# Kernel tuning notes

Measured on AMD Instinct MI355X. Metric: run time of the kernel, lower is better.

## Reference

```python
import jax, jax.numpy as jnp
import numpy as np
from jax import lax

B, N, T, E, HE, HD, NE = 512, 100, 100, 128, 64, 256, 512
BETA = 0.25


def setup_inputs() -> dict:
    key = jax.random.key(0)
    ks = jax.random.split(key, 16)
    f32 = jnp.float32
    x = jax.random.normal(ks[0], (B, N, T), f32)
    traj_mask = (jax.random.uniform(ks[1], (B, N, T)) > 0.1).astype(f32)
    instance_mask = (jax.random.uniform(ks[2], (B, N)) > 0.2).astype(f32)

    def w_init(k, shape, fan_in):
        return (jax.random.normal(k, shape, f32) / np.sqrt(fan_in)).astype(f32)

    params = dict(
        conv1_w=w_init(ks[3], (HE, 2, 3), 2 * 3), conv1_b=jnp.zeros((HE,), f32),
        conv2_w=w_init(ks[4], (HE, HE, 3), HE * 3), conv2_b=jnp.zeros((HE,), f32),
        lat_w=w_init(ks[5], (E, HE), HE), lat_b=jnp.zeros((E,), f32),
        codebook=(jax.random.uniform(ks[6], (NE, E), f32) * 2.0 - 1.0) / NE,
        d1_w=w_init(ks[7], (HD, E), E), d1_b=jnp.zeros((HD,), f32),
        d2_w=w_init(ks[8], (HD, HD), HD), d2_b=jnp.zeros((HD,), f32),
        d3_w=w_init(ks[9], (T, HD), HD), d3_b=jnp.zeros((T,), f32),
    )
    return {"x": x, "traj_mask": traj_mask, "instance_mask": instance_mask, **params}


def _conv1d(h, w, b):
    # h: (M, C_in, L), w: (C_out, C_in, K) -> (M, C_out, L), padding=1 == SAME for K=3
    y = lax.conv_general_dilated(h, w, (1,), 'SAME', dimension_numbers=('NCH', 'OIH', 'NCH'))
    return jax.nn.relu(y + b[None, :, None])


def reference(x, traj_mask, instance_mask, conv1_w, conv1_b, conv2_w, conv2_b,
              lat_w, lat_b, codebook, d1_w, d1_b, d2_w, d2_b, d3_w, d3_b):
    b, n, t = x.shape
    steps = t // 2
    im = instance_mask[..., None]  # (B,N,1)

    # ---- encode (masked input) ----
    x_in = x * traj_mask * im
    h = x_in.reshape(b * n, steps, 2).transpose(0, 2, 1)  # (M, 2, steps)
    h = _conv1d(h, conv1_w, conv1_b)
    h = _conv1d(h, conv2_w, conv2_b)
    h = h.mean(axis=-1)                                   # (M, HE)
    z = (h @ lat_w.T + lat_b).reshape(b, n, -1)           # (B, N, E)
    z = z * im

    # ---- vector quantize (nbooks=1), quant_prop=1.0 ----
    zf = z.reshape(-1, z.shape[-1])                       # (M, E)
    d = ((zf * zf).sum(-1, keepdims=True)
         - 2.0 * zf @ codebook.T
         + (codebook * codebook).sum(-1))                 # (M, NE)
    idx = jnp.argmin(d, axis=-1)                          # (M,)
    zq = codebook[idx]                                    # (M, E) gather
    sg = lax.stop_gradient
    vq_loss = (BETA * jnp.mean((zf - sg(zq)) ** 2, -1)
               + jnp.mean((sg(zf) - zq) ** 2, -1)).reshape(b, n)
    zq = zf + sg(zq - zf)                                 # straight-through
    z_q = zq.reshape(b, n, -1)

    # ---- apply instance mask to VQ outputs ----
    denom = jnp.maximum(instance_mask.sum(), 1.0)
    vq_reduced = (vq_loss * instance_mask).sum() / denom
    indices = idx.reshape(b, n, 1)
    indices = jnp.where(im > 0, indices, jnp.full_like(indices, -1))
    z_q = z_q * im

    # ---- decode ----
    h2 = jax.nn.relu(z_q.reshape(b * n, -1) @ d1_w.T + d1_b)
    h2 = jax.nn.relu(h2 @ d2_w.T + d2_b)
    x_hat = (h2 @ d3_w.T + d3_b).reshape(b, n, t)

    # ---- masked reconstruction loss ----
    recon_w = im * traj_mask
    recon_loss = (((x_hat - x) ** 2) * recon_w).sum() / jnp.maximum(recon_w.sum(), 1.0)
    return x_hat, recon_loss, vq_reduced, indices
```

## Files before the change

### kernel.cpp

```cpp
#include <hip/hip_runtime.h>
#include <stdint.h>

typedef unsigned long long u64;
typedef unsigned short ushort_t;
typedef __attribute__((ext_vector_type(8))) short short8;
typedef __attribute__((ext_vector_type(8))) _Float16 half8;
typedef __attribute__((ext_vector_type(16))) float f32x16;


#define WS_RNP0     0ll
#define WS_RNP1     51200ll
#define WS_ZHI      102400ll
#define WS_ZLO      3379200ll
#define WS_ENCBHI   6656000ll
#define WS_ENCBLO   6662144ll
#define WS_CBHI     6668288ll
#define WS_CBLO     6701056ll
#define WS_CBNORM   6733824ll
#define WS_D1F      6734336ll
#define WS_D2F      6750720ll
#define WS_D3F      6783488ll
#define WS_ACCUMS   6799872ll
#define WS_GBEST    6799880ll
#define WS_RED      6902280ll

__device__ __host__ inline ushort_t bf16_rn(float v) {
  unsigned u = __float_as_uint(v);
  unsigned r = (u + 0x7fffu + ((u >> 16) & 1u)) >> 16;
  return (ushort_t)r;
}
union h2u { _Float16 h; unsigned short u; };
union s2h { short8 s; half8 h; };

__device__ inline unsigned pk2_bf16(float a, float b) {
  unsigned r;
  asm("v_cvt_pk_bf16_f32 %0, %1, %2" : "=v"(r) : "v"(a), "v"(b));
  return r;
}

__device__ inline int rowfn(int r, int half) { return (r & 3) + 8*(r >> 2) + 4*half; }

#define MFMA_BF16 __builtin_amdgcn_mfma_f32_32x32x16_bf16

__global__ __launch_bounds__(256) void prep_kernel(
    const float* __restrict__ w2, const float* __restrict__ cb,
    const float* __restrict__ d1w, const float* __restrict__ d2w,
    const float* __restrict__ d3w,
    ushort_t* __restrict__ ebhi, ushort_t* __restrict__ eblo,
    ushort_t* __restrict__ cbhi, ushort_t* __restrict__ cblo,
    ushort_t* __restrict__ d1f, ushort_t* __restrict__ d2f,
    ushort_t* __restrict__ d3f, float* __restrict__ cbnorm)
{
  const int total = 12288 + 65536 + 32768 + 65536 + 32768 + 512;
  for (int i = blockIdx.x*256 + threadIdx.x; i < total; i += gridDim.x*256) {
    int idx = i;
    if (idx < 12288) {
      int j = idx & 7, l6 = (idx >> 3) & 63, f = idx >> 9;
      int kt = f & 3, ntt = (f >> 2) & 1, t = f >> 3;
      int oc = ntt*32 + (l6 & 31);
      int ic = kt*16 + (l6 >> 5)*8 + j;
      float v = w2[(oc*64 + ic)*3 + t];
      ushort_t hi = bf16_rn(v);
      float hf = __uint_as_float(((unsigned)hi) << 16);
      ebhi[idx] = hi; eblo[idx] = bf16_rn(v - hf); continue;
    }
    idx -= 12288;
    if (idx < 65536) {
      int j = idx & 7, l6 = (idx >> 3) & 63, f = idx >> 9;
      int kt = f & 7, ntg = f >> 3;
      int k = kt*16 + (l6 >> 5)*8 + j;
      int n = ntg*32 + (l6 & 31);
      float v = cb[n*128 + k] * 512.0f;
      h2u a, b; a.h = (_Float16)v;
      b.h = (_Float16)(v - (float)a.h);
      cbhi[idx] = a.u; cblo[idx] = b.u; continue;
    }
    idx -= 65536;
    if (idx < 32768) {
      int j = idx & 7, l6 = (idx >> 3) & 63, f = idx >> 9;
      int kt = f & 7, ntg = f >> 3;
      int k = kt*16 + (l6 >> 5)*8 + j;
      int n = ntg*32 + (l6 & 31);
      d1f[idx] = bf16_rn(d1w[n*128 + k]); continue;
    }
    idx -= 32768;
    if (idx < 65536) {
      int j = idx & 7, l6 = (idx >> 3) & 63, f = idx >> 9;
      int kt = f & 15, ntg = f >> 4;
      int k = kt*16 + (l6 >> 5)*8 + j;
      int n = ntg*32 + (l6 & 31);
      d2f[idx] = bf16_rn(d2w[n*256 + k]); continue;
    }
    idx -= 65536;
    if (idx < 32768) {
      int j = idx & 7, l6 = (idx >> 3) & 63, f = idx >> 9;
      int kt = f & 15, ntg = f >> 4;
      int k = kt*16 + (l6 >> 5)*8 + j;
      int n = ntg*32 + (l6 & 31);
      d3f[idx] = (n < 100) ? bf16_rn(d3w[n*256 + k]) : (ushort_t)0; continue;
    }
    idx -= 32768;
    { double s = 0.0; const float* c = cb + idx*128;
      for (int e = 0; e < 128; ++e) { double v = (double)c[e]; s += v*v; }
      cbnorm[idx] = (float)s; }
  }
}

__global__ __launch_bounds__(256, 3) void encoder_kernel(
    const float* __restrict__ x, const float* __restrict__ tm,
    const float* __restrict__ imask,
    const float* w1, const float* b1,
    const ushort_t* __restrict__ ebhi, const ushort_t* __restrict__ eblo,
    const float* b2, float* __restrict__ red)
{
  __shared__ ushort_t s_H[4][52*128];
  const int tid  = threadIdx.x;
  const int wv   = __builtin_amdgcn_readfirstlane((int)(tid >> 6));
  const int lane = tid & 63;
  const int ln31 = lane & 31, half = lane >> 5;
  const long m   = (long)blockIdx.x*4 + wv;
  const float imv = imask[m];
  ushort_t* Hw  = s_H[wv];

  {
    const int p = (lane < 50) ? lane : 0;
    const long xb = m*100 + 2*p;
    const float2 x0v = *(const float2*)(x + xb);
    const float2 t0v = *(const float2*)(tm + xb);
    float2 xmv = {0.f, 0.f}, tmv = {0.f, 0.f};
    float2 xpv = {0.f, 0.f}, tpv = {0.f, 0.f};
    if (p > 0)  { xmv = *(const float2*)(x + xb - 2); tmv = *(const float2*)(tm + xb - 2); }
    if (p < 49) { xpv = *(const float2*)(x + xb + 2); tpv = *(const float2*)(tm + xb + 2); }
    const float a0 = xmv.x*tmv.x, c0 = xmv.y*tmv.y;
    const float a1 = x0v.x*t0v.x, c1 = x0v.y*t0v.y;
    const float a2 = xpv.x*tpv.x, c2 = xpv.y*tpv.y;
    const int row = lane + 1;
    const int sw  = ((row & 7) << 4) | (((row >> 3) & 1) << 7);
    char* rbase = (char*)(Hw + row*128);
    #pragma unroll
    for (int g = 0; g < 4; ++g) {
      unsigned hi8[8], lo8[8];
      #pragma unroll
      for (int pr = 0; pr < 8; ++pr) {
        const int o = g*16 + pr*2;
        const float* wA = w1 + (long)o*6;
        const float* wB = wA + 6;
        float sA = 0.f, sB = 0.f;
        sA = fmaf(wA[0], a0, sA); sA = fmaf(wA[1], a1, sA); sA = fmaf(wA[2], a2, sA);
        sA = fmaf(wA[3], c0, sA); sA = fmaf(wA[4], c1, sA); sA = fmaf(wA[5], c2, sA);
        sB = fmaf(wB[0], a0, sB); sB = fmaf(wB[1], a1, sB); sB = fmaf(wB[2], a2, sB);
        sB = fmaf(wB[3], c0, sB); sB = fmaf(wB[4], c1, sB); sB = fmaf(wB[5], c2, sB);
        const float hA = fmaxf(fmaf(imv, sA, b1[o]),     0.f);
        const float hB = fmaxf(fmaf(imv, sB, b1[o + 1]), 0.f);
        const unsigned h = pk2_bf16(hA, hB);
        const float ha = __uint_as_float(h << 16);
        const float hb = __uint_as_float(h & 0xffff0000u);
        lo8[pr] = pk2_bf16(hA - ha, hB - hb);
        hi8[pr] = h;
      }
      if (lane < 50) {
        *(short8*)(rbase + ((g*32)        ^ sw)) = *(short8*)&hi8[0];
        *(short8*)(rbase + ((g*32 + 16)   ^ sw)) = *(short8*)&hi8[4];
        *(short8*)(rbase + ((g*32 + 128)  ^ sw)) = *(short8*)&lo8[0];
        *(short8*)(rbase + ((g*32 + 144)  ^ sw)) = *(short8*)&lo8[4];
      }
    }
    if (lane == 50 || lane == 51) {
      const int zr = (lane == 50) ? 0 : 51;
      short8 z8 = {};
      short8* d = (short8*)(Hw + zr*128);
      #pragma unroll
      for (int i = 0; i < 16; ++i) d[i] = z8;
    }
  }
  asm volatile("s_waitcnt lgkmcnt(0)" ::: "memory");
  __builtin_amdgcn_sched_barrier(0);

  f32x16 acc00, acc01, acc10, acc11;
  #pragma unroll
  for (int q = 0; q < 16; ++q) { acc00[q] = 0.f; acc01[q] = 0.f; acc10[q] = 0.f; acc11[q] = 0.f; }
  {
    const short8* bh8 = (const short8*)ebhi;
    const short8* bl8 = (const short8*)eblo;
    for (int t = 0; t < 3; ++t) {
      const int r0 = ln31 + t;
      int r1 = 32 + ln31 + t;
      if (r1 > 51) r1 = 51;
      const int sw0 = ((r0 & 7) << 4) | (((r0 >> 3) & 1) << 7);
      const int sw1 = ((r1 & 7) << 4) | (((r1 >> 3) & 1) << 7);
      const char* b0p = (const char*)(Hw + r0*128);
      const char* b1p = (const char*)(Hw + r1*128);
      #pragma unroll
      for (int kt = 0; kt < 4; ++kt) {
        const int f0 = (t*2 + 0)*4 + kt;
        const int f1 = (t*2 + 1)*4 + kt;
        const int offh = kt*32 + half*16;
        const short8 Bh0 = bh8[f0*64 + lane], Bl0 = bl8[f0*64 + lane];
        const short8 Bh1 = bh8[f1*64 + lane], Bl1 = bl8[f1*64 + lane];
        const short8 ah0 = *(const short8*)(b0p + (offh ^ sw0));
        const short8 al0 = *(const short8*)(b0p + ((offh + 128) ^ sw0));
        const short8 ah1 = *(const short8*)(b1p + (offh ^ sw1));
        const short8 al1 = *(const short8*)(b1p + ((offh + 128) ^ sw1));
        acc00 = MFMA_BF16(ah0, Bh0, acc00, 0, 0, 0);
        acc00 = MFMA_BF16(ah0, Bl0, acc00, 0, 0, 0);
        acc00 = MFMA_BF16(al0, Bh0, acc00, 0, 0, 0);
        acc01 = MFMA_BF16(ah0, Bh1, acc01, 0, 0, 0);
        acc01 = MFMA_BF16(ah0, Bl1, acc01, 0, 0, 0);
        acc01 = MFMA_BF16(al0, Bh1, acc01, 0, 0, 0);
        acc10 = MFMA_BF16(ah1, Bh0, acc10, 0, 0, 0);
        acc10 = MFMA_BF16(ah1, Bl0, acc10, 0, 0, 0);
        acc10 = MFMA_BF16(al1, Bh0, acc10, 0, 0, 0);
        acc11 = MFMA_BF16(ah1, Bh1, acc11, 0, 0, 0);
        acc11 = MFMA_BF16(ah1, Bl1, acc11, 0, 0, 0);
        acc11 = MFMA_BF16(al1, Bh1, acc11, 0, 0, 0);
      }
    }
  }

  {
    const float bv0 = b2[ln31];
    const float bv1 = b2[32 + ln31];
    float s0 = 0.f, s1 = 0.f;
    #pragma unroll
    for (int r = 0; r < 16; ++r) {
      s0 += fmaxf(acc00[r] + bv0, 0.f);
      s1 += fmaxf(acc01[r] + bv1, 0.f);
      const int mpos = 32 + rowfn(r, half);
      const float v10 = fmaxf(acc10[r] + bv0, 0.f);
      const float v11 = fmaxf(acc11[r] + bv1, 0.f);
      if (mpos < 50) { s0 += v10; s1 += v11; }
    }
    s0 += __shfl_xor(s0, 32);
    s1 += __shfl_xor(s1, 32);
    if (half == 0) {
      red[m*64 + ln31]      = s0;
      red[m*64 + 32 + ln31] = s1;
    }
  }
}

__global__ __launch_bounds__(256, 4) void latent_kernel(
    const float* __restrict__ red, const float* __restrict__ imask,
    const float* __restrict__ latw, const float* __restrict__ latb,
    ushort_t* __restrict__ zhi, ushort_t* __restrict__ zlo,
    float* __restrict__ rnp0, float* __restrict__ rnp1)
{
  __shared__ float s_r[64*64];
  __shared__ float s_im[64];
  const int tid = threadIdx.x;
  const long m0 = (long)blockIdx.x * 64;
  {
    const int r = tid >> 2, seg = tid & 3;
    const float4* src = (const float4*)(red + (m0 + r)*64 + seg*16);
    float4* dst = (float4*)(s_r + r*64 + seg*16);
    dst[0] = src[0]; dst[1] = src[1]; dst[2] = src[2]; dst[3] = src[3];
  }
  if (tid < 64) s_im[tid] = imask[m0 + tid];
  __syncthreads();

  const int e = tid & 127, mh = tid >> 7;
  const int lane = tid & 63;
  float4 W[16];
  const float4* wp = (const float4*)(latw + (long)e*64);
  #pragma unroll
  for (int q = 0; q < 16; ++q) W[q] = wp[q];
  const float lb = latb[e];

  for (int i = 0; i < 32; ++i) {
    const int ml = mh*32 + i;
    const float4* rp = (const float4*)(s_r + ml*64);
    float a = 0.f;
    #pragma unroll
    for (int q = 0; q < 16; ++q) {
      const float4 r4 = rp[q];
      a = fmaf(W[q].x, r4.x, a); a = fmaf(W[q].y, r4.y, a);
      a = fmaf(W[q].z, r4.z, a); a = fmaf(W[q].w, r4.w, a);
    }
    const float z = fmaf(0.02f, a, lb) * s_im[ml];
    h2u zh, zl; zh.h = (_Float16)z; zl.h = (_Float16)(z - (float)zh.h);
    const long mg = m0 + ml;
    zhi[mg*128 + e] = zh.u;
    zlo[mg*128 + e] = zl.u;
    float v = z*z;
    #pragma unroll
    for (int off = 32; off > 0; off >>= 1) v += __shfl_down(v, off);
    if (lane == 0) { if (e < 64) rnp0[mg] = v; else rnp1[mg] = v; }
  }
}

__global__ __launch_bounds__(256) void vq_kernel(
    const ushort_t* __restrict__ zhi, const ushort_t* __restrict__ zlo,
    const ushort_t* __restrict__ cbhi, const ushort_t* __restrict__ cblo,
    const float* __restrict__ rnp0, const float* __restrict__ rnp1,
    const float* __restrict__ cbnorm, u64* __restrict__ gbest)
{
  __shared__ ushort_t s_ah[32*136];
  __shared__ ushort_t s_al[32*136];
  __shared__ float s_rn[32];
  __shared__ u64 s_best[32];
  const int tid = threadIdx.x;
  const int m0 = blockIdx.x * 32;
  {
    const short8* gh = (const short8*)(zhi + (long)m0*128);
    const short8* gl = (const short8*)(zlo + (long)m0*128);
    const int row = tid >> 3, c8 = (tid & 7)*2;
    ((short8*)s_ah)[row*17 + c8]     = gh[tid*2];
    ((short8*)s_ah)[row*17 + c8 + 1] = gh[tid*2 + 1];
    ((short8*)s_al)[row*17 + c8]     = gl[tid*2];
    ((short8*)s_al)[row*17 + c8 + 1] = gl[tid*2 + 1];
  }
  if (tid < 32) { s_rn[tid] = rnp0[m0 + tid] + rnp1[m0 + tid]; s_best[tid] = ~0ULL; }
  __syncthreads();

  const int wv = tid >> 6, lane = tid & 63;
  const int ln31 = lane & 31, half = lane >> 5;
  float rnv[16];
  #pragma unroll
  for (int r = 0; r < 16; ++r) rnv[r] = s_rn[rowfn(r, half)];

  u64 best[16];
  #pragma unroll
  for (int r = 0; r < 16; ++r) best[r] = ~0ULL;

  const short8* ch8 = (const short8*)cbhi;
  const short8* cl8 = (const short8*)cblo;
  for (int ct = 0; ct < 4; ++ct) {
    const int ntg = wv*4 + ct;
    half8 Bh[8], Bl[8];
    #pragma unroll
    for (int kt = 0; kt < 8; ++kt) {
      s2h a, b;
      a.s = ch8[(ntg*8 + kt)*64 + lane];
      b.s = cl8[(ntg*8 + kt)*64 + lane];
      Bh[kt] = a.h; Bl[kt] = b.h;
    }
    f32x16 acc;
    #pragma unroll
    for (int q = 0; q < 16; ++q) acc[q] = 0.f;
    const int base8 = ln31*17 + half;
    #pragma unroll
    for (int kt = 0; kt < 8; ++kt) {
      s2h ah, al;
      ah.s = ((const short8*)s_ah)[base8 + kt*2];
      al.s = ((const short8*)s_al)[base8 + kt*2];
      acc = __builtin_amdgcn_mfma_f32_32x32x16_f16(ah.h, Bh[kt], acc, 0, 0, 0);
      acc = __builtin_amdgcn_mfma_f32_32x32x16_f16(ah.h, Bl[kt], acc, 0, 0, 0);
      acc = __builtin_amdgcn_mfma_f32_32x32x16_f16(al.h, Bh[kt], acc, 0, 0, 0);
    }
    const int code = ntg*32 + ln31;
    const float nrm = cbnorm[code];
    #pragma unroll
    for (int r = 0; r < 16; ++r) {
      const float t = fmaf(-0.00390625f, acc[r], rnv[r]);
      const float d = t + nrm;
      const u64 pk = ((u64)__float_as_uint(d) << 32) | (u64)(unsigned)code;
      if (pk < best[r]) best[r] = pk;
    }
  }
  #pragma unroll
  for (int r = 0; r < 16; ++r) atomicMin(&s_best[rowfn(r, half)], best[r]);
  __syncthreads();
  if (tid < 32) gbest[m0 + tid] = s_best[tid];
}

__global__ __launch_bounds__(256, 2) void decoder_kernel(
    const float* __restrict__ cb, const u64* __restrict__ gbest,
    const float* __restrict__ imask,
    const ushort_t* __restrict__ d1frag, const float* __restrict__ d1b,
    const ushort_t* __restrict__ d2frag, const float* __restrict__ d2b,
    const ushort_t* __restrict__ d3frag, const float* __restrict__ d3b,
    const float* __restrict__ x, const float* __restrict__ tm,
    float* __restrict__ xhat, float* __restrict__ out_idx,
    float* __restrict__ accums)
{
  __shared__ ushort_t s_u[64*264];
  __shared__ ushort_t s_h1[64*264];
  __shared__ int s_idx[64];
  __shared__ float s_act[64];
  __shared__ float s_p[4], s_w[4];
  const int tid = threadIdx.x;
  const long m0 = (long)blockIdx.x * 64;

  if (tid < 64) {
    const u64 pk = gbest[m0 + tid];
    const int ii = (int)(unsigned)(pk & 0xffffffffULL);
    const float dd = __uint_as_float((unsigned)(pk >> 32));
    const float imv = imask[m0 + tid];
    s_idx[tid] = ii; s_act[tid] = imv;
    out_idx[m0 + tid] = (imv > 0.f) ? (float)ii : -1.0f;
    float vqp = 1.25f * dd * (1.0f/128.0f) * imv;
    float sim = imv;
    #pragma unroll
    for (int off = 32; off > 0; off >>= 1) {
      vqp += __shfl_down(vqp, off); sim += __shfl_down(sim, off);
    }
    if (tid == 0) { atomicAdd(&accums[1], vqp); atomicAdd(&accums[3], sim); }
  }
  __syncthreads();
  {
    const int row = tid >> 2, seg = tid & 3;
    const float4* src = (const float4*)(cb + (long)s_idx[row]*128 + seg*32);
    const float im = s_act[row];
    ushort_t tmp[32];
    #pragma unroll
    for (int q = 0; q < 8; ++q) {
      const float4 v = src[q];
      tmp[q*4+0] = bf16_rn(v.x*im); tmp[q*4+1] = bf16_rn(v.y*im);
      tmp[q*4+2] = bf16_rn(v.z*im); tmp[q*4+3] = bf16_rn(v.w*im);
    }
    short8* dst = (short8*)(s_u + row*136 + seg*32);
    #pragma unroll
    for (int q = 0; q < 4; ++q) dst[q] = *(short8*)&tmp[q*8];
  }
  __syncthreads();

  const int wv = tid >> 6, lane = tid & 63;
  const int ln31 = lane & 31, half = lane >> 5;

  {
    const short8* bf = (const short8*)d1frag;
    #pragma unroll
    for (int nti = 0; nti < 2; ++nti) {
      const int ntg = wv + nti*4;
      short8 B[8];
      #pragma unroll
      for (int kt = 0; kt < 8; ++kt) B[kt] = bf[(ntg*8 + kt)*64 + lane];
      const float bv = d1b[ntg*32 + ln31];
      #pragma unroll
      for (int mtl = 0; mtl < 2; ++mtl) {
        f32x16 acc;
        #pragma unroll
        for (int q = 0; q < 16; ++q) acc[q] = 0.f;
        const int base8 = (mtl*32 + ln31)*17 + half;
        #pragma unroll
        for (int kt = 0; kt < 8; ++kt) {
          const short8 a = ((const short8*)s_u)[base8 + kt*2];
          acc = MFMA_BF16(a, B[kt], acc, 0, 0, 0);
        }
        const int col = ntg*32 + ln31;
        #pragma unroll
        for (int r = 0; r < 16; ++r) {
          const int row = mtl*32 + rowfn(r, half);
          s_h1[row*264 + col] = bf16_rn(fmaxf(acc[r] + bv, 0.f));
        }
      }
    }
  }
  __syncthreads();

  {
    const short8* bf = (const short8*)d2frag;
    #pragma unroll
    for (int nti = 0; nti < 2; ++nti) {
      const int ntg = wv + nti*4;
      short8 B[16];
      #pragma unroll
      for (int kt = 0; kt < 16; ++kt) B[kt] = bf[(ntg*16 + kt)*64 + lane];
      const float bv = d2b[ntg*32 + ln31];
      #pragma unroll
      for (int mtl = 0; mtl < 2; ++mtl) {
        f32x16 acc;
        #pragma unroll
        for (int q = 0; q < 16; ++q) acc[q] = 0.f;
        const int base8 = (mtl*32 + ln31)*33 + half;
        #pragma unroll
        for (int kt = 0; kt < 16; ++kt) {
          const short8 a = ((const short8*)s_h1)[base8 + kt*2];
          acc = MFMA_BF16(a, B[kt], acc, 0, 0, 0);
        }
        const int col = ntg*32 + ln31;
        #pragma unroll
        for (int r = 0; r < 16; ++r) {
          const int row = mtl*32 + rowfn(r, half);
          s_u[row*264 + col] = bf16_rn(fmaxf(acc[r] + bv, 0.f));
        }
      }
    }
  }
  __syncthreads();

  {
    const short8* bf = (const short8*)d3frag;
    const int ntg = wv;
    short8 B[16];
    #pragma unroll
    for (int kt = 0; kt < 16; ++kt) B[kt] = bf[(ntg*16 + kt)*64 + lane];
    const int col = ntg*32 + ln31;
    const float bv = (col < 100) ? d3b[col] : 0.f;
    float part = 0.f, wsum = 0.f;
    #pragma unroll
    for (int mtl = 0; mtl < 2; ++mtl) {
      f32x16 acc;
      #pragma unroll
      for (int q = 0; q < 16; ++q) acc[q] = 0.f;
      const int base8 = (mtl*32 + ln31)*33 + half;
      #pragma unroll
      for (int kt = 0; kt < 16; ++kt) {
        const short8 a = ((const short8*)s_u)[base8 + kt*2];
        acc = MFMA_BF16(a, B[kt], acc, 0, 0, 0);
      }
      if (col < 100) {
        #pragma unroll
        for (int r = 0; r < 16; ++r) {
          const long row = m0 + mtl*32 + rowfn(r, half);
          const float xh = acc[r] + bv;
          xhat[row*100 + col] = xh;
          const float wgt = imask[row] * tm[row*100 + col];
          const float df = xh - x[row*100 + col];
          part = fmaf(df*df, wgt, part);
          wsum += wgt;
        }
      }
    }
    #pragma unroll
    for (int off = 32; off > 0; off >>= 1) {
      part += __shfl_down(part, off); wsum += __shfl_down(wsum, off);
    }
    if (lane == 0) { s_p[wv] = part; s_w[wv] = wsum; }
    __syncthreads();
    if (tid == 0) {
      atomicAdd(&accums[0], s_p[0]+s_p[1]+s_p[2]+s_p[3]);
      atomicAdd(&accums[2], s_w[0]+s_w[1]+s_w[2]+s_w[3]);
    }
  }
}

__global__ void finalize_kernel(const float* __restrict__ accums, float* __restrict__ out) {
  if (threadIdx.x == 0 && blockIdx.x == 0) {
    out[5120000] = accums[0] / fmaxf(accums[2], 1.0f);
    out[5120001] = accums[1] / fmaxf(accums[3], 1.0f);
  }
}

extern "C" void kernel_launch(void* const* d_in, const int* in_sizes, int n_in,
                              void* d_out, int out_size, void* d_ws, size_t ws_size,
                              hipStream_t stream)
{
  (void)in_sizes; (void)n_in; (void)out_size; (void)ws_size;
  const float* x     = (const float*)d_in[0];
  const float* tmsk  = (const float*)d_in[1];
  const float* imask = (const float*)d_in[2];
  const float* w1    = (const float*)d_in[3];
  const float* b1    = (const float*)d_in[4];
  const float* w2    = (const float*)d_in[5];
  const float* b2    = (const float*)d_in[6];
  const float* latw  = (const float*)d_in[7];
  const float* latb  = (const float*)d_in[8];
  const float* cb    = (const float*)d_in[9];
  const float* d1w   = (const float*)d_in[10];
  const float* d1b   = (const float*)d_in[11];
  const float* d2w   = (const float*)d_in[12];
  const float* d2b   = (const float*)d_in[13];
  const float* d3w   = (const float*)d_in[14];
  const float* d3b   = (const float*)d_in[15];
  float* out = (float*)d_out;
  float* ws  = (float*)d_ws;

  float*    rnp0   = ws + WS_RNP0;
  float*    rnp1   = ws + WS_RNP1;
  ushort_t* zhi    = (ushort_t*)(ws + WS_ZHI);
  ushort_t* zlo    = (ushort_t*)(ws + WS_ZLO);
  ushort_t* ebhi   = (ushort_t*)(ws + WS_ENCBHI);
  ushort_t* eblo   = (ushort_t*)(ws + WS_ENCBLO);
  ushort_t* cbhi   = (ushort_t*)(ws + WS_CBHI);
  ushort_t* cblo   = (ushort_t*)(ws + WS_CBLO);
  float*    cbnorm = ws + WS_CBNORM;
  ushort_t* d1f    = (ushort_t*)(ws + WS_D1F);
  ushort_t* d2f    = (ushort_t*)(ws + WS_D2F);
  ushort_t* d3f    = (ushort_t*)(ws + WS_D3F);
  float*    accums = ws + WS_ACCUMS;
  u64*      gbest  = (u64*)(ws + WS_GBEST);
  float*    red    = ws + WS_RED;
  float* xhat    = out;
  float* out_idx = out + 5120002;

  hipMemsetAsync(accums, 0, 8*sizeof(float), stream);

  prep_kernel<<<512, 256, 0, stream>>>(w2, cb, d1w, d2w, d3w,
                                       ebhi, eblo, cbhi, cblo, d1f, d2f, d3f, cbnorm);
  encoder_kernel<<<12800, 256, 0, stream>>>(x, tmsk, imask, w1, b1, ebhi, eblo, b2, red);
  latent_kernel<<<800, 256, 0, stream>>>(red, imask, latw, latb, zhi, zlo, rnp0, rnp1);
  vq_kernel<<<1600, 256, 0, stream>>>(zhi, zlo, cbhi, cblo, rnp0, rnp1, cbnorm, gbest);
  decoder_kernel<<<800, 256, 0, stream>>>(cb, gbest, imask, d1f, d1b, d2f, d2b,
                                          d3f, d3b, x, tmsk, xhat, out_idx, accums);
  finalize_kernel<<<1, 64, 0, stream>>>(accums, out);
}
```

Measured before the change: 437.0 us.

## Fuse latent projection, VQ search and decoder into one kernel

Merges the latent, vq and decoder kernels into a single vqdec kernel that keeps z hi/lo halves, row norms and argmin results in shared memory, reusing the decoder's LDS buffers. This removes global round trips for zhi/zlo/rnp/gbest and two kernel launches. The trade-off is that the VQ stage now runs with 64-row blocks at 800 blocks instead of 1600 blocks of 32 rows, and the kernel's occupancy is bounded by the decoder's register and LDS usage.

```diff
diff --git a/kernel.cpp b/kernel.cpp
--- a/kernel.cpp
+++ b/kernel.cpp
@@ -8,10 +8,6 @@
 typedef __attribute__((ext_vector_type(16))) float f32x16;
 
 
-#define WS_RNP0     0ll
-#define WS_RNP1     51200ll
-#define WS_ZHI      102400ll
-#define WS_ZLO      3379200ll
 #define WS_ENCBHI   6656000ll
 #define WS_ENCBLO   6662144ll
 #define WS_CBHI     6668288ll
@@ -21,7 +17,6 @@
 #define WS_D2F      6750720ll
 #define WS_D3F      6783488ll
 #define WS_ACCUMS   6799872ll
-#define WS_GBEST    6799880ll
 #define WS_RED      6902280ll
 
 __device__ __host__ inline ushort_t bf16_rn(float v) {
@@ -41,6 +36,7 @@
 __device__ inline int rowfn(int r, int half) { return (r & 3) + 8*(r >> 2) + 4*half; }
 
 #define MFMA_BF16 __builtin_amdgcn_mfma_f32_32x32x16_bf16
+#define MFMA_F16  __builtin_amdgcn_mfma_f32_32x32x16_f16
 
 __global__ __launch_bounds__(256) void prep_kernel(
     const float* __restrict__ w2, const float* __restrict__ cb,
@@ -239,133 +235,11 @@
   }
 }
 
-__global__ __launch_bounds__(256, 4) void latent_kernel(
+__global__ __launch_bounds__(256, 2) void vqdec_kernel(
     const float* __restrict__ red, const float* __restrict__ imask,
     const float* __restrict__ latw, const float* __restrict__ latb,
-    ushort_t* __restrict__ zhi, ushort_t* __restrict__ zlo,
-    float* __restrict__ rnp0, float* __restrict__ rnp1)
-{
-  __shared__ float s_r[64*64];
-  __shared__ float s_im[64];
-  const int tid = threadIdx.x;
-  const long m0 = (long)blockIdx.x * 64;
-  {
-    const int r = tid >> 2, seg = tid & 3;
-    const float4* src = (const float4*)(red + (m0 + r)*64 + seg*16);
-    float4* dst = (float4*)(s_r + r*64 + seg*16);
-    dst[0] = src[0]; dst[1] = src[1]; dst[2] = src[2]; dst[3] = src[3];
-  }
-  if (tid < 64) s_im[tid] = imask[m0 + tid];
-  __syncthreads();
-
-  const int e = tid & 127, mh = tid >> 7;
-  const int lane = tid & 63;
-  float4 W[16];
-  const float4* wp = (const float4*)(latw + (long)e*64);
-  #pragma unroll
-  for (int q = 0; q < 16; ++q) W[q] = wp[q];
-  const float lb = latb[e];
-
-  for (int i = 0; i < 32; ++i) {
-    const int ml = mh*32 + i;
-    const float4* rp = (const float4*)(s_r + ml*64);
-    float a = 0.f;
-    #pragma unroll
-    for (int q = 0; q < 16; ++q) {
-      const float4 r4 = rp[q];
-      a = fmaf(W[q].x, r4.x, a); a = fmaf(W[q].y, r4.y, a);
-      a = fmaf(W[q].z, r4.z, a); a = fmaf(W[q].w, r4.w, a);
-    }
-    const float z = fmaf(0.02f, a, lb) * s_im[ml];
-    h2u zh, zl; zh.h = (_Float16)z; zl.h = (_Float16)(z - (float)zh.h);
-    const long mg = m0 + ml;
-    zhi[mg*128 + e] = zh.u;
-    zlo[mg*128 + e] = zl.u;
-    float v = z*z;
-    #pragma unroll
-    for (int off = 32; off > 0; off >>= 1) v += __shfl_down(v, off);
-    if (lane == 0) { if (e < 64) rnp0[mg] = v; else rnp1[mg] = v; }
-  }
-}
-
-__global__ __launch_bounds__(256) void vq_kernel(
-    const ushort_t* __restrict__ zhi, const ushort_t* __restrict__ zlo,
     const ushort_t* __restrict__ cbhi, const ushort_t* __restrict__ cblo,
-    const float* __restrict__ rnp0, const float* __restrict__ rnp1,
-    const float* __restrict__ cbnorm, u64* __restrict__ gbest)
-{
-  __shared__ ushort_t s_ah[32*136];
-  __shared__ ushort_t s_al[32*136];
-  __shared__ float s_rn[32];
-  __shared__ u64 s_best[32];
-  const int tid = threadIdx.x;
-  const int m0 = blockIdx.x * 32;
-  {
-    const short8* gh = (const short8*)(zhi + (long)m0*128);
-    const short8* gl = (const short8*)(zlo + (long)m0*128);
-    const int row = tid >> 3, c8 = (tid & 7)*2;
-    ((short8*)s_ah)[row*17 + c8]     = gh[tid*2];
-    ((short8*)s_ah)[row*17 + c8 + 1] = gh[tid*2 + 1];
-    ((short8*)s_al)[row*17 + c8]     = gl[tid*2];
-    ((short8*)s_al)[row*17 + c8 + 1] = gl[tid*2 + 1];
-  }
-  if (tid < 32) { s_rn[tid] = rnp0[m0 + tid] + rnp1[m0 + tid]; s_best[tid] = ~0ULL; }
-  __syncthreads();
-
-  const int wv = tid >> 6, lane = tid & 63;
-  const int ln31 = lane & 31, half = lane >> 5;
-  float rnv[16];
-  #pragma unroll
-  for (int r = 0; r < 16; ++r) rnv[r] = s_rn[rowfn(r, half)];
-
-  u64 best[16];
-  #pragma unroll
-  for (int r = 0; r < 16; ++r) best[r] = ~0ULL;
-
-  const short8* ch8 = (const short8*)cbhi;
-  const short8* cl8 = (const short8*)cblo;
-  for (int ct = 0; ct < 4; ++ct) {
-    const int ntg = wv*4 + ct;
-    half8 Bh[8], Bl[8];
-    #pragma unroll
-    for (int kt = 0; kt < 8; ++kt) {
-      s2h a, b;
-      a.s = ch8[(ntg*8 + kt)*64 + lane];
-      b.s = cl8[(ntg*8 + kt)*64 + lane];
-      Bh[kt] = a.h; Bl[kt] = b.h;
-    }
-    f32x16 acc;
-    #pragma unroll
-    for (int q = 0; q < 16; ++q) acc[q] = 0.f;
-    const int base8 = ln31*17 + half;
-    #pragma unroll
-    for (int kt = 0; kt < 8; ++kt) {
-      s2h ah, al;
-      ah.s = ((const short8*)s_ah)[base8 + kt*2];
-      al.s = ((const short8*)s_al)[base8 + kt*2];
-      acc = __builtin_amdgcn_mfma_f32_32x32x16_f16(ah.h, Bh[kt], acc, 0, 0, 0);
-      acc = __builtin_amdgcn_mfma_f32_32x32x16_f16(ah.h, Bl[kt], acc, 0, 0, 0);
-      acc = __builtin_amdgcn_mfma_f32_32x32x16_f16(al.h, Bh[kt], acc, 0, 0, 0);
-    }
-    const int code = ntg*32 + ln31;
-    const float nrm = cbnorm[code];
-    #pragma unroll
-    for (int r = 0; r < 16; ++r) {
-      const float t = fmaf(-0.00390625f, acc[r], rnv[r]);
-      const float d = t + nrm;
-      const u64 pk = ((u64)__float_as_uint(d) << 32) | (u64)(unsigned)code;
-      if (pk < best[r]) best[r] = pk;
-    }
-  }
-  #pragma unroll
-  for (int r = 0; r < 16; ++r) atomicMin(&s_best[rowfn(r, half)], best[r]);
-  __syncthreads();
-  if (tid < 32) gbest[m0 + tid] = s_best[tid];
-}
-
-__global__ __launch_bounds__(256, 2) void decoder_kernel(
-    const float* __restrict__ cb, const u64* __restrict__ gbest,
-    const float* __restrict__ imask,
+    const float* __restrict__ cbnorm, const float* __restrict__ cb,
     const ushort_t* __restrict__ d1frag, const float* __restrict__ d1b,
     const ushort_t* __restrict__ d2frag, const float* __restrict__ d2b,
     const ushort_t* __restrict__ d3frag, const float* __restrict__ d3b,
@@ -373,19 +247,123 @@
     float* __restrict__ xhat, float* __restrict__ out_idx,
     float* __restrict__ accums)
 {
-  __shared__ ushort_t s_u[64*264];
-  __shared__ ushort_t s_h1[64*264];
+  __shared__ __attribute__((aligned(16))) ushort_t s_reg1[64*264];
+  __shared__ __attribute__((aligned(16))) ushort_t s_reg2[64*264];
   __shared__ int s_idx[64];
   __shared__ float s_act[64];
+  __shared__ float s_rn0[64], s_rn1[64];
+  __shared__ u64 s_best[64];
+  __shared__ float s_im[64];
   __shared__ float s_p[4], s_w[4];
+
+  float*    s_r  = (float*)s_reg1;
+  ushort_t* s_al = s_reg1 + 8192;
+  ushort_t* s_ah = s_reg2;
+  ushort_t* s_u  = s_reg1;
+  ushort_t* s_h1 = s_reg2;
+
   const int tid = threadIdx.x;
   const long m0 = (long)blockIdx.x * 64;
+  const int wv = tid >> 6, lane = tid & 63;
+  const int ln31 = lane & 31, half = lane >> 5;
+
+  {
+    const int r = tid >> 2, seg = tid & 3;
+    const float4* src = (const float4*)(red + (m0 + r)*64 + seg*16);
+    float4* dst = (float4*)(s_r + r*64 + seg*16);
+    dst[0] = src[0]; dst[1] = src[1]; dst[2] = src[2]; dst[3] = src[3];
+  }
+  if (tid < 64) { s_im[tid] = imask[m0 + tid]; s_best[tid] = ~0ULL; }
+  __syncthreads();
+
+  {
+    const int e = tid & 127, mh = tid >> 7;
+    float4 W[16];
+    const float4* wp = (const float4*)(latw + (long)e*64);
+    #pragma unroll
+    for (int q = 0; q < 16; ++q) W[q] = wp[q];
+    const float lb = latb[e];
+    for (int i = 0; i < 32; ++i) {
+      const int ml = mh*32 + i;
+      const float4* rp = (const float4*)(s_r + ml*64);
+      float a = 0.f;
+      #pragma unroll
+      for (int q = 0; q < 16; ++q) {
+        const float4 r4 = rp[q];
+        a = fmaf(W[q].x, r4.x, a); a = fmaf(W[q].y, r4.y, a);
+        a = fmaf(W[q].z, r4.z, a); a = fmaf(W[q].w, r4.w, a);
+      }
+      const float z = fmaf(0.02f, a, lb) * s_im[ml];
+      h2u zh, zl; zh.h = (_Float16)z; zl.h = (_Float16)(z - (float)zh.h);
+      s_ah[ml*136 + e] = zh.u;
+      s_al[ml*136 + e] = zl.u;
+      float v = z*z;
+      #pragma unroll
+      for (int off = 32; off > 0; off >>= 1) v += __shfl_down(v, off);
+      if (lane == 0) { if (e < 64) s_rn0[ml] = v; else s_rn1[ml] = v; }
+    }
+  }
+  __syncthreads();
+
+  {
+    const short8* ch8 = (const short8*)cbhi;
+    const short8* cl8 = (const short8*)cblo;
+    #pragma unroll
+    for (int mtl = 0; mtl < 2; ++mtl) {
+      float rnv[16];
+      #pragma unroll
+      for (int r = 0; r < 16; ++r) {
+        const int g = mtl*32 + rowfn(r, half);
+        rnv[r] = s_rn0[g] + s_rn1[g];
+      }
+      u64 best[16];
+      #pragma unroll
+      for (int r = 0; r < 16; ++r) best[r] = ~0ULL;
+      for (int ct = 0; ct < 4; ++ct) {
+        const int ntg = wv*4 + ct;
+        half8 Bh[8], Bl[8];
+        #pragma unroll
+        for (int kt = 0; kt < 8; ++kt) {
+          s2h a, b;
+          a.s = ch8[(ntg*8 + kt)*64 + lane];
+          b.s = cl8[(ntg*8 + kt)*64 + lane];
+          Bh[kt] = a.h; Bl[kt] = b.h;
+        }
+        f32x16 acc;
+        #pragma unroll
+        for (int q = 0; q < 16; ++q) acc[q] = 0.f;
+        const int base8 = (mtl*32 + ln31)*17 + half;
+        #pragma unroll
+        for (int kt = 0; kt < 8; ++kt) {
+          s2h ah, al;
+          ah.s = ((const short8*)s_ah)[base8 + kt*2];
+          al.s = ((const short8*)s_al)[base8 + kt*2];
+          acc = MFMA_F16(ah.h, Bh[kt], acc, 0, 0, 0);
+          acc = MFMA_F16(ah.h, Bl[kt], acc, 0, 0, 0);
+          acc = MFMA_F16(al.h, Bh[kt], acc, 0, 0, 0);
+        }
+        const int code = ntg*32 + ln31;
+        const float nrm = cbnorm[code];
+        #pragma unroll
+        for (int r = 0; r < 16; ++r) {
+          const float t = fmaf(-0.00390625f, acc[r], rnv[r]);
+          const float d = t + nrm;
+          const u64 pk = ((u64)__float_as_uint(d) << 32) | (u64)(unsigned)code;
+          if (pk < best[r]) best[r] = pk;
+        }
+      }
+      #pragma unroll
+      for (int r = 0; r < 16; ++r)
+        atomicMin(&s_best[mtl*32 + rowfn(r, half)], best[r]);
+    }
+  }
+  __syncthreads();
 
   if (tid < 64) {
-    const u64 pk = gbest[m0 + tid];
+    const u64 pk = s_best[tid];
     const int ii = (int)(unsigned)(pk & 0xffffffffULL);
     const float dd = __uint_as_float((unsigned)(pk >> 32));
-    const float imv = imask[m0 + tid];
+    const float imv = s_im[tid];
     s_idx[tid] = ii; s_act[tid] = imv;
     out_idx[m0 + tid] = (imv > 0.f) ? (float)ii : -1.0f;
     float vqp = 1.25f * dd * (1.0f/128.0f) * imv;
@@ -413,9 +391,6 @@
     for (int q = 0; q < 4; ++q) dst[q] = *(short8*)&tmp[q*8];
   }
   __syncthreads();
-
-  const int wv = tid >> 6, lane = tid & 63;
-  const int ln31 = lane & 31, half = lane >> 5;
 
   {
     const short8* bf = (const short8*)d1frag;
@@ -556,10 +531,6 @@
   float* out = (float*)d_out;
   float* ws  = (float*)d_ws;
 
-  float*    rnp0   = ws + WS_RNP0;
-  float*    rnp1   = ws + WS_RNP1;
-  ushort_t* zhi    = (ushort_t*)(ws + WS_ZHI);
-  ushort_t* zlo    = (ushort_t*)(ws + WS_ZLO);
   ushort_t* ebhi   = (ushort_t*)(ws + WS_ENCBHI);
   ushort_t* eblo   = (ushort_t*)(ws + WS_ENCBLO);
   ushort_t* cbhi   = (ushort_t*)(ws + WS_CBHI);
@@ -569,7 +540,6 @@
   ushort_t* d2f    = (ushort_t*)(ws + WS_D2F);
   ushort_t* d3f    = (ushort_t*)(ws + WS_D3F);
   float*    accums = ws + WS_ACCUMS;
-  u64*      gbest  = (u64*)(ws + WS_GBEST);
   float*    red    = ws + WS_RED;
   float* xhat    = out;
   float* out_idx = out + 5120002;
@@ -579,9 +549,8 @@
   prep_kernel<<<512, 256, 0, stream>>>(w2, cb, d1w, d2w, d3w,
                                        ebhi, eblo, cbhi, cblo, d1f, d2f, d3f, cbnorm);
   encoder_kernel<<<12800, 256, 0, stream>>>(x, tmsk, imask, w1, b1, ebhi, eblo, b2, red);
-  latent_kernel<<<800, 256, 0, stream>>>(red, imask, latw, latb, zhi, zlo, rnp0, rnp1);
-  vq_kernel<<<1600, 256, 0, stream>>>(zhi, zlo, cbhi, cblo, rnp0, rnp1, cbnorm, gbest);
-  decoder_kernel<<<800, 256, 0, stream>>>(cb, gbest, imask, d1f, d1b, d2f, d2b,
-                                          d3f, d3b, x, tmsk, xhat, out_idx, accums);
+  vqdec_kernel<<<800, 256, 0, stream>>>(red, imask, latw, latb, cbhi, cblo, cbnorm, cb,
+                                        d1f, d1b, d2f, d2b, d3f, d3b, x, tmsk,
+                                        xhat, out_idx, accums);
   finalize_kernel<<<1, 64, 0, stream>>>(accums, out);
 }
```

After: 428.6 us. No clear change (-1.9%).
